# Optimization experiments

Hardware: AMD Instinct MI355X
Metric: run time of the kernel (lower is better)

Reference implementation:

```python
import jax, jax.numpy as jnp
import numpy as np

N = 100000   # total atoms in the batch
E = 400000   # directed edges (bonds both directions)
F = 11       # raw atom feature dim (Linear(11, vector_dim))
D = 512      # vector_dim
L = 5        # num_conv_layers
G = 2048     # number of molecules (graphs) in the batch


def setup_inputs() -> dict:
    key = jax.random.key(0)
    k = jax.random.split(key, 6)
    x = jax.random.uniform(k[0], (N, F), dtype=jnp.float32)  # nonneg counts-like features
    edge_index = jax.random.randint(k[1], (2, E), 0, N, dtype=jnp.int32)
    batch = jnp.sort(jax.random.randint(k[2], (N,), 0, G, dtype=jnp.int32))
    exp_W = jax.random.normal(k[3], (F, D), dtype=jnp.float32) * (1.0 / np.sqrt(F))
    exp_b = jnp.zeros((D,), dtype=jnp.float32)
    gcn_W = jax.random.normal(k[4], (L, D, D), dtype=jnp.float32) * (1.0 / np.sqrt(D))
    gcn_b = jnp.zeros((L, D), dtype=jnp.float32)
    return {"x": x, "edge_index": edge_index, "batch": batch,
            "exp_W": exp_W, "exp_b": exp_b, "gcn_W": gcn_W, "gcn_b": gcn_b}


def reference(x, edge_index, batch, exp_W, exp_b, gcn_W, gcn_b):
    # GraphEmbedding.forward (eval mode: dropout = identity)
    src, dst = edge_index[0], edge_index[1]
    h = jnp.log(x + 1.0) @ exp_W + exp_b  # expansion Linear(11, D)  -> [N, D]

    # GCN normalization with improved=True: self-loop weight 2.0
    # deg_i = sum of incoming edge weights (1.0) + 2.0 self-loop
    ones_e = jnp.ones((E,), dtype=h.dtype)
    deg = jax.ops.segment_sum(ones_e, dst, num_segments=N) + 2.0
    dinv = jax.lax.rsqrt(deg)              # deg >= 2, always finite
    enorm = dinv[src] * dinv[dst]          # per-edge norm (weight 1.0)
    self_norm = 2.0 * dinv * dinv          # self-loop norm (weight 2.0)

    for l in range(L):
        xw = h @ gcn_W[l]                                   # [N, D]
        msg = enorm[:, None] * xw[src]                      # gather + scale, [E, D]
        agg = jax.ops.segment_sum(msg, dst, num_segments=N)  # scatter-add
        agg = agg + self_norm[:, None] * xw + gcn_b[l]
        h = h + jax.nn.relu(agg)                            # residual + relu (dropout off)

    # global_add_pool over molecules
    return jax.ops.segment_sum(h, batch, num_segments=G)    # [G, D]
```

## Files before the change

### kernel.cpp

```cpp
#include <hip/hip_runtime.h>
#include <hip/hip_bf16.h>
#include <stdint.h>

typedef __attribute__((ext_vector_type(8))) short bf16x8;
typedef __attribute__((ext_vector_type(4))) float f32x4;
typedef unsigned short ushort_t;
typedef unsigned int uint_t;

__device__ __forceinline__ unsigned short f2bf(float f) {
  unsigned u = __float_as_uint(f);
  u += 0x7fffu + ((u >> 16) & 1u);
  return (unsigned short)(u >> 16);
}
__device__ __forceinline__ float bf2f(unsigned u16) {
  return __uint_as_float(u16 << 16);
}

__global__ void k_zero(int* __restrict__ p, int n) {
  int i = blockIdx.x * blockDim.x + threadIdx.x;
  if (i < n) p[i] = 0;
}

__global__ void k_prep_w(const float* __restrict__ W, ushort_t* __restrict__ Wt, int total) {
  int idx = blockIdx.x * blockDim.x + threadIdx.x;
  if (idx >= total) return;
  int j   = idx & 7;
  int col = (idx >> 3) & 127;
  int kg  = (idx >> 10) & 3;
  int kt  = (idx >> 12) & 15;
  int nt  = (idx >> 16) & 3;
  int l   = idx >> 18;
  int k = kt * 32 + kg * 8 + j;
  int n = nt * 128 + col;
  Wt[idx] = f2bf(W[((size_t)(l * 512 + k)) * 512 + n]);
}

__global__ __launch_bounds__(256) void k_expand(const float* __restrict__ x,
                                                const float* __restrict__ eW,
                                                const float* __restrict__ eb,
                                                ushort_t* __restrict__ h, int N) {
  const int wid = (blockIdx.x * 256 + threadIdx.x) >> 6;
  const int nw = (gridDim.x * 256) >> 6;
  const int l = threadIdx.x & 63;

  float wf[11][8];
  float bias[8];
#pragma unroll
  for (int f = 0; f < 11; ++f) {
    float4 a = *(const float4*)&eW[f * 512 + l * 8];
    float4 b = *(const float4*)&eW[f * 512 + l * 8 + 4];
    wf[f][0] = a.x; wf[f][1] = a.y; wf[f][2] = a.z; wf[f][3] = a.w;
    wf[f][4] = b.x; wf[f][5] = b.y; wf[f][6] = b.z; wf[f][7] = b.w;
  }
  {
    float4 a = *(const float4*)&eb[l * 8];
    float4 b = *(const float4*)&eb[l * 8 + 4];
    bias[0] = a.x; bias[1] = a.y; bias[2] = a.z; bias[3] = a.w;
    bias[4] = b.x; bias[5] = b.y; bias[6] = b.z; bias[7] = b.w;
  }

  for (int n = wid; n < N; n += nw) {
    float xv = (l < 11) ? x[(size_t)n * 11 + l] : 0.f;
    float lx = log1pf(xv);
    float acc[8];
#pragma unroll
    for (int j = 0; j < 8; ++j) acc[j] = bias[j];
#pragma unroll
    for (int f = 0; f < 11; ++f) {
      float c = __shfl(lx, f, 64);
#pragma unroll
      for (int j = 0; j < 8; ++j) acc[j] += c * wf[f][j];
    }
    uint4 pu;
    pu.x = (uint_t)f2bf(acc[0]) | ((uint_t)f2bf(acc[1]) << 16);
    pu.y = (uint_t)f2bf(acc[2]) | ((uint_t)f2bf(acc[3]) << 16);
    pu.z = (uint_t)f2bf(acc[4]) | ((uint_t)f2bf(acc[5]) << 16);
    pu.w = (uint_t)f2bf(acc[6]) | ((uint_t)f2bf(acc[7]) << 16);
    *(uint4*)(h + (size_t)n * 512 + l * 8) = pu;
  }
}

__global__ void k_deg(const int* __restrict__ dst, int* __restrict__ deg, int E) {
  int e = blockIdx.x * blockDim.x + threadIdx.x;
  if (e < E) atomicAdd(&deg[dst[e]], 1);
}

__global__ void k_dinv(const int* __restrict__ deg, float* __restrict__ dinv,
                       float* __restrict__ selfn, int N) {
  int n = blockIdx.x * blockDim.x + threadIdx.x;
  if (n >= N) return;
  float d = (float)deg[n] + 2.0f;
  dinv[n] = rsqrtf(d);
  selfn[n] = 2.0f / d;
}

__global__ void k_scan_a(const int* __restrict__ deg, int* __restrict__ off,
                         int* __restrict__ bsum, int N) {
  __shared__ int sd[256];
  int t = threadIdx.x;
  int i0 = blockIdx.x * 1024 + t * 4;
  int d[4];
#pragma unroll
  for (int j = 0; j < 4; ++j) d[j] = (i0 + j < N) ? deg[i0 + j] : 0;
  int ts = d[0] + d[1] + d[2] + d[3];
  sd[t] = ts;
  __syncthreads();
  for (int o = 1; o < 256; o <<= 1) {
    int v = (t >= o) ? sd[t - o] : 0;
    __syncthreads();
    sd[t] += v;
    __syncthreads();
  }
  int incl = sd[t];
  int run = incl - ts;
#pragma unroll
  for (int j = 0; j < 4; ++j) {
    if (i0 + j < N) off[i0 + j] = run;
    run += d[j];
  }
  if (t == 255) bsum[blockIdx.x] = incl;
}

__global__ void k_scan_b(const int* __restrict__ bsum, int* __restrict__ bpre, int nb,
                         int* __restrict__ off, int N, int E) {
  __shared__ int sd[256];
  int t = threadIdx.x;
  int v = (t < nb) ? bsum[t] : 0;
  sd[t] = v;
  __syncthreads();
  for (int o = 1; o < 256; o <<= 1) {
    int u = (t >= o) ? sd[t - o] : 0;
    __syncthreads();
    sd[t] += u;
    __syncthreads();
  }
  if (t < nb) bpre[t] = sd[t] - v;
  if (t == 0) off[N] = E;
}

__global__ void k_scan_c(int* __restrict__ off, const int* __restrict__ bpre, int N) {
  int i = blockIdx.x * blockDim.x + threadIdx.x;
  if (i < N) off[i] += bpre[i >> 10];
}

__global__ void k_fill(const int* __restrict__ src, const int* __restrict__ dst,
                       const int* __restrict__ off, int* __restrict__ cur,
                       int* __restrict__ ssrc, int E) {
  int e = blockIdx.x * blockDim.x + threadIdx.x;
  if (e >= E) return;
  int t = dst[e];
  int p = atomicAdd(&cur[t], 1);
  ssrc[off[t] + p] = src[e];
}

__global__ __launch_bounds__(256) void k_agg2(const ushort_t* __restrict__ h,
                                              ushort_t* __restrict__ s,
                                              const int* __restrict__ off,
                                              const int* __restrict__ ssrc,
                                              const float* __restrict__ dinv,
                                              const float* __restrict__ selfn, int N) {
  const int wid = (blockIdx.x * 256 + threadIdx.x) >> 6;
  const int nw = (gridDim.x * 256) >> 6;
  const int l = threadIdx.x & 63;

  for (int n = wid; n < N; n += nw) {
    int s0 = off[n], s1 = off[n + 1];
    float dn = dinv[n];
    float sn = selfn[n];
    float acc[8];
    {
      uint4 u = *(const uint4*)(h + (size_t)n * 512 + l * 8);
      acc[0] = sn * bf2f(u.x & 0xffffu); acc[1] = sn * bf2f(u.x >> 16);
      acc[2] = sn * bf2f(u.y & 0xffffu); acc[3] = sn * bf2f(u.y >> 16);
      acc[4] = sn * bf2f(u.z & 0xffffu); acc[5] = sn * bf2f(u.z >> 16);
      acc[6] = sn * bf2f(u.w & 0xffffu); acc[7] = sn * bf2f(u.w >> 16);
    }
    for (int i = s0; i < s1; ++i) {
      int sv = ssrc[i];
      float w = dn * dinv[sv];
      uint4 u = *(const uint4*)(h + (size_t)sv * 512 + l * 8);
      acc[0] += w * bf2f(u.x & 0xffffu); acc[1] += w * bf2f(u.x >> 16);
      acc[2] += w * bf2f(u.y & 0xffffu); acc[3] += w * bf2f(u.y >> 16);
      acc[4] += w * bf2f(u.z & 0xffffu); acc[5] += w * bf2f(u.z >> 16);
      acc[6] += w * bf2f(u.w & 0xffffu); acc[7] += w * bf2f(u.w >> 16);
    }
    uint4 pu;
    pu.x = (uint_t)f2bf(acc[0]) | ((uint_t)f2bf(acc[1]) << 16);
    pu.y = (uint_t)f2bf(acc[2]) | ((uint_t)f2bf(acc[3]) << 16);
    pu.z = (uint_t)f2bf(acc[4]) | ((uint_t)f2bf(acc[5]) << 16);
    pu.w = (uint_t)f2bf(acc[6]) | ((uint_t)f2bf(acc[7]) << 16);
    *(uint4*)(s + (size_t)n * 512 + l * 8) = pu;
  }
}

__global__ __launch_bounds__(256) void k_gemm(const ushort_t* __restrict__ s,
                                              const ushort_t* __restrict__ Wt,
                                              const float* __restrict__ gbl,
                                              ushort_t* __restrict__ h, int N) {
  __shared__ alignas(16) short Alds[4 * 128 * 8];
  __shared__ alignas(16) short Blds[4 * 128 * 8];
  const int tid = threadIdx.x;
  const int m0 = blockIdx.x * 128;
  const int nt = blockIdx.y;
  const int wv = tid >> 6, ln = tid & 63;
  const int wrow = wv >> 1, wcol = wv & 1;
  const int l15 = ln & 15, l4 = ln >> 4;

  f32x4 acc[4][4];
#pragma unroll
  for (int i = 0; i < 4; ++i)
#pragma unroll
    for (int j = 0; j < 4; ++j) acc[i][j] = (f32x4){0.f, 0.f, 0.f, 0.f};

  const int r = tid >> 1, hh = tid & 1;
  const int grow = m0 + r;
  const bool valid = grow < N;
  const ushort_t* srow = s + (size_t)grow * 512 + hh * 16;
  const int abase0 = ((hh * 2 + 0) * 128 + r) * 8;
  const int abase1 = ((hh * 2 + 1) * 128 + r) * 8;

  for (int kt = 0; kt < 16; ++kt) {
    __syncthreads();
    {
      const ushort_t* wt = Wt + (((size_t)nt * 16 + kt) << 12);
      const ushort_t* g1 = wt + ((wv * 64 + ln) << 3);
      const ushort_t* g2 = g1 + 2048;
      __builtin_amdgcn_global_load_lds(
          (const __attribute__((address_space(1))) unsigned int*)g1,
          (__attribute__((address_space(3))) unsigned int*)&Blds[(wv * 64) << 3], 16, 0, 0);
      __builtin_amdgcn_global_load_lds(
          (const __attribute__((address_space(1))) unsigned int*)g2,
          (__attribute__((address_space(3))) unsigned int*)&Blds[(256 + wv * 64) << 3], 16, 0, 0);
    }
    {
      bf16x8 v0, v1;
      if (valid) {
        v0 = ((const bf16x8*)(srow + kt * 32))[0];
        v1 = ((const bf16x8*)(srow + kt * 32))[1];
      } else {
        v0 = (bf16x8){0, 0, 0, 0, 0, 0, 0, 0};
        v1 = v0;
      }
      *(bf16x8*)&Alds[abase0] = v0;
      *(bf16x8*)&Alds[abase1] = v1;
    }
    __syncthreads();
    bf16x8 a[4], b[4];
#pragma unroll
    for (int i = 0; i < 4; ++i) {
      a[i] = *(const bf16x8*)&Alds[(l4 * 128 + wrow * 64 + i * 16 + l15) * 8];
      b[i] = *(const bf16x8*)&Blds[(l4 * 128 + wcol * 64 + i * 16 + l15) * 8];
    }
#pragma unroll
    for (int i = 0; i < 4; ++i)
#pragma unroll
      for (int j = 0; j < 4; ++j)
        acc[i][j] = __builtin_amdgcn_mfma_f32_16x16x32_bf16(a[i], b[j], acc[i][j], 0, 0, 0);
  }

  float bj[4];
#pragma unroll
  for (int j = 0; j < 4; ++j)
    bj[j] = gbl[nt * 128 + wcol * 64 + j * 16 + l15];

#pragma unroll
  for (int i = 0; i < 4; ++i) {
    int row0 = m0 + wrow * 64 + i * 16 + l4 * 4;
#pragma unroll
    for (int v = 0; v < 4; ++v) {
      int row = row0 + v;
      if (row < N) {
#pragma unroll
        for (int j = 0; j < 4; ++j) {
          int col = nt * 128 + wcol * 64 + j * 16 + l15;
          size_t idx = (size_t)row * 512 + col;
          float hv = bf2f(h[idx]);
          hv += fmaxf(acc[i][j][v] + bj[j], 0.f);
          h[idx] = f2bf(hv);
        }
      }
    }
  }
}

__device__ __forceinline__ int lbound(const int* a, int n, int v) {
  int lo = 0, hi = n;
  while (lo < hi) {
    int m = (lo + hi) >> 1;
    if (a[m] < v) lo = m + 1; else hi = m;
  }
  return lo;
}

__global__ __launch_bounds__(256) void k_pool(const ushort_t* __restrict__ h,
                                              const int* __restrict__ batch,
                                              float* __restrict__ out, int N) {
  __shared__ float red[4 * 512];
  int g = blockIdx.x;
  int t = threadIdx.x;
  int w = t >> 6, l = t & 63;
  int start = lbound(batch, N, g);
  int end = lbound(batch, N, g + 1);
  float acc[8];
#pragma unroll
  for (int j = 0; j < 8; ++j) acc[j] = 0.f;
  for (int n = start + w; n < end; n += 4) {
    uint4 u = *(const uint4*)(h + (size_t)n * 512 + l * 8);
    acc[0] += bf2f(u.x & 0xffffu); acc[1] += bf2f(u.x >> 16);
    acc[2] += bf2f(u.y & 0xffffu); acc[3] += bf2f(u.y >> 16);
    acc[4] += bf2f(u.z & 0xffffu); acc[5] += bf2f(u.z >> 16);
    acc[6] += bf2f(u.w & 0xffffu); acc[7] += bf2f(u.w >> 16);
  }
#pragma unroll
  for (int j = 0; j < 8; ++j) red[w * 512 + l * 8 + j] = acc[j];
  __syncthreads();
  if (t < 128) {
    float4 sv = make_float4(0.f, 0.f, 0.f, 0.f);
#pragma unroll
    for (int ww = 0; ww < 4; ++ww) {
      float4 v = *(const float4*)&red[ww * 512 + t * 4];
      sv.x += v.x; sv.y += v.y; sv.z += v.z; sv.w += v.w;
    }
    *(float4*)&out[(size_t)g * 512 + t * 4] = sv;
  }
}

extern "C" void kernel_launch(void* const* d_in, const int* in_sizes, int n_in,
                              void* d_out, int out_size, void* d_ws, size_t ws_size,
                              hipStream_t stream) {
  const float* x  = (const float*)d_in[0];
  const int* ei   = (const int*)d_in[1];
  const int* batch= (const int*)d_in[2];
  const float* eW = (const float*)d_in[3];
  const float* eb = (const float*)d_in[4];
  const float* gW = (const float*)d_in[5];
  const float* gb = (const float*)d_in[6];
  float* out = (float*)d_out;

  const int N = in_sizes[0] / 11;
  const int E = in_sizes[1] / 2;
  const int G = out_size / 512;
  const int L = in_sizes[5] / (512 * 512);

  const int* src = ei;
  const int* dst = ei + E;

  size_t nd = (size_t)N * 512;
  char* p = (char*)d_ws;
  auto carve = [&](size_t bytes) {
    char* q = p;
    p += (bytes + 255) & ~(size_t)255;
    return q;
  };
  ushort_t* h         = (ushort_t*)carve(nd * 2);
  ushort_t* s         = (ushort_t*)carve(nd * 2);
  ushort_t* Wt        = (ushort_t*)carve((size_t)L * 512 * 512 * 2);
  int* deg            = (int*)carve((size_t)N * 4);
  float* dinv         = (float*)carve((size_t)N * 4);
  float* selfn        = (float*)carve((size_t)N * 4);
  int* off            = (int*)carve(((size_t)N + 1) * 4);
  int* cur            = (int*)carve((size_t)N * 4);
  int* ssrc           = (int*)carve((size_t)E * 4);
  int* bsum           = (int*)carve(1024);
  int* bpre           = (int*)carve(1024);

  k_zero<<<(N + 255) / 256, 256, 0, stream>>>(deg, N);
  k_zero<<<(N + 255) / 256, 256, 0, stream>>>(cur, N);

  int totW = L * 512 * 512;
  k_prep_w<<<(totW + 255) / 256, 256, 0, stream>>>(gW, Wt, totW);
  k_expand<<<2048, 256, 0, stream>>>(x, eW, eb, h, N);
  k_deg<<<(E + 255) / 256, 256, 0, stream>>>(dst, deg, E);
  k_dinv<<<(N + 255) / 256, 256, 0, stream>>>(deg, dinv, selfn, N);
  int nb = (N + 1023) / 1024;
  k_scan_a<<<nb, 256, 0, stream>>>(deg, off, bsum, N);
  k_scan_b<<<1, 256, 0, stream>>>(bsum, bpre, nb, off, N, E);
  k_scan_c<<<(N + 255) / 256, 256, 0, stream>>>(off, bpre, N);
  k_fill<<<(E + 255) / 256, 256, 0, stream>>>(src, dst, off, cur, ssrc, E);

  dim3 ggrid((N + 127) / 128, 4);
  for (int l = 0; l < L; ++l) {
    k_agg2<<<2048, 256, 0, stream>>>(h, s, off, ssrc, dinv, selfn, N);
    k_gemm<<<ggrid, 256, 0, stream>>>(s, Wt + (size_t)l * 512 * 512,
                                      gb + (size_t)l * 512, h, N);
  }
  k_pool<<<G, 256, 0, stream>>>(h, batch, out, N);
}
```

Before: 1.172 ms.

## Interleave two nodes in aggregation, async-load A tiles, stage GEMM epilogue via LDS

The aggregation kernel now has each wavefront handle two destination nodes at once, interleaving their neighbor gathers so more independent loads are in flight. The GEMM loads A tiles with direct global-to-LDS loads in a row-major layout, replacing register staging. Its epilogue writes accumulators to shared memory and then performs coalesced 16-byte read-modify-write of h instead of scattered 2-byte accesses. The costs are extra synchronisation in the epilogue, a different LDS read pattern for A that may cause bank conflicts, and clamped row indices for out-of-range rows.

```diff
diff --git a/kernel.cpp b/kernel.cpp
--- a/kernel.cpp
+++ b/kernel.cpp
@@ -14,6 +14,20 @@
 }
 __device__ __forceinline__ float bf2f(unsigned u16) {
   return __uint_as_float(u16 << 16);
+}
+__device__ __forceinline__ void fma8(float* a, uint4 u, float w) {
+  a[0] += w * bf2f(u.x & 0xffffu); a[1] += w * bf2f(u.x >> 16);
+  a[2] += w * bf2f(u.y & 0xffffu); a[3] += w * bf2f(u.y >> 16);
+  a[4] += w * bf2f(u.z & 0xffffu); a[5] += w * bf2f(u.z >> 16);
+  a[6] += w * bf2f(u.w & 0xffffu); a[7] += w * bf2f(u.w >> 16);
+}
+__device__ __forceinline__ uint4 pack8u(const float* a) {
+  uint4 p;
+  p.x = (uint_t)f2bf(a[0]) | ((uint_t)f2bf(a[1]) << 16);
+  p.y = (uint_t)f2bf(a[2]) | ((uint_t)f2bf(a[3]) << 16);
+  p.z = (uint_t)f2bf(a[4]) | ((uint_t)f2bf(a[5]) << 16);
+  p.w = (uint_t)f2bf(a[6]) | ((uint_t)f2bf(a[7]) << 16);
+  return p;
 }
 
 __global__ void k_zero(int* __restrict__ p, int n) {
@@ -71,12 +85,7 @@
 #pragma unroll
       for (int j = 0; j < 8; ++j) acc[j] += c * wf[f][j];
     }
-    uint4 pu;
-    pu.x = (uint_t)f2bf(acc[0]) | ((uint_t)f2bf(acc[1]) << 16);
-    pu.y = (uint_t)f2bf(acc[2]) | ((uint_t)f2bf(acc[3]) << 16);
-    pu.z = (uint_t)f2bf(acc[4]) | ((uint_t)f2bf(acc[5]) << 16);
-    pu.w = (uint_t)f2bf(acc[6]) | ((uint_t)f2bf(acc[7]) << 16);
-    *(uint4*)(h + (size_t)n * 512 + l * 8) = pu;
+    *(uint4*)(h + (size_t)n * 512 + l * 8) = pack8u(acc);
   }
 }
 
@@ -163,33 +172,49 @@
   const int nw = (gridDim.x * 256) >> 6;
   const int l = threadIdx.x & 63;
 
-  for (int n = wid; n < N; n += nw) {
-    int s0 = off[n], s1 = off[n + 1];
-    float dn = dinv[n];
-    float sn = selfn[n];
-    float acc[8];
+  for (int n0 = wid * 2; n0 < N; n0 += nw * 2) {
+    const int n1 = n0 + 1;
+    const bool v1 = n1 < N;
+    int i0 = off[n0], e0 = off[n0 + 1];
+    int i1 = v1 ? e0 : 0, e1 = v1 ? off[n1 + 1] : 0;
+    float dn0 = dinv[n0], dn1 = v1 ? dinv[n1] : 0.f;
+    float a0[8], a1[8];
     {
-      uint4 u = *(const uint4*)(h + (size_t)n * 512 + l * 8);
-      acc[0] = sn * bf2f(u.x & 0xffffu); acc[1] = sn * bf2f(u.x >> 16);
-      acc[2] = sn * bf2f(u.y & 0xffffu); acc[3] = sn * bf2f(u.y >> 16);
-      acc[4] = sn * bf2f(u.z & 0xffffu); acc[5] = sn * bf2f(u.z >> 16);
-      acc[6] = sn * bf2f(u.w & 0xffffu); acc[7] = sn * bf2f(u.w >> 16);
-    }
-    for (int i = s0; i < s1; ++i) {
-      int sv = ssrc[i];
-      float w = dn * dinv[sv];
-      uint4 u = *(const uint4*)(h + (size_t)sv * 512 + l * 8);
-      acc[0] += w * bf2f(u.x & 0xffffu); acc[1] += w * bf2f(u.x >> 16);
-      acc[2] += w * bf2f(u.y & 0xffffu); acc[3] += w * bf2f(u.y >> 16);
-      acc[4] += w * bf2f(u.z & 0xffffu); acc[5] += w * bf2f(u.z >> 16);
-      acc[6] += w * bf2f(u.w & 0xffffu); acc[7] += w * bf2f(u.w >> 16);
-    }
-    uint4 pu;
-    pu.x = (uint_t)f2bf(acc[0]) | ((uint_t)f2bf(acc[1]) << 16);
-    pu.y = (uint_t)f2bf(acc[2]) | ((uint_t)f2bf(acc[3]) << 16);
-    pu.z = (uint_t)f2bf(acc[4]) | ((uint_t)f2bf(acc[5]) << 16);
-    pu.w = (uint_t)f2bf(acc[6]) | ((uint_t)f2bf(acc[7]) << 16);
-    *(uint4*)(s + (size_t)n * 512 + l * 8) = pu;
+      uint4 u = *(const uint4*)(h + (size_t)n0 * 512 + l * 8);
+      float sn = selfn[n0];
+      a0[0] = sn * bf2f(u.x & 0xffffu); a0[1] = sn * bf2f(u.x >> 16);
+      a0[2] = sn * bf2f(u.y & 0xffffu); a0[3] = sn * bf2f(u.y >> 16);
+      a0[4] = sn * bf2f(u.z & 0xffffu); a0[5] = sn * bf2f(u.z >> 16);
+      a0[6] = sn * bf2f(u.w & 0xffffu); a0[7] = sn * bf2f(u.w >> 16);
+    }
+#pragma unroll
+    for (int j = 0; j < 8; ++j) a1[j] = 0.f;
+    if (v1) {
+      uint4 u = *(const uint4*)(h + (size_t)n1 * 512 + l * 8);
+      fma8(a1, u, selfn[n1]);
+    }
+    while (i0 < e0 && i1 < e1) {
+      int m0 = ssrc[i0++], m1 = ssrc[i1++];
+      float w0 = dn0 * dinv[m0], w1 = dn1 * dinv[m1];
+      uint4 u0 = *(const uint4*)(h + (size_t)m0 * 512 + l * 8);
+      uint4 u1 = *(const uint4*)(h + (size_t)m1 * 512 + l * 8);
+      fma8(a0, u0, w0);
+      fma8(a1, u1, w1);
+    }
+    while (i0 < e0) {
+      int m0 = ssrc[i0++];
+      float w0 = dn0 * dinv[m0];
+      uint4 u0 = *(const uint4*)(h + (size_t)m0 * 512 + l * 8);
+      fma8(a0, u0, w0);
+    }
+    while (i1 < e1) {
+      int m1 = ssrc[i1++];
+      float w1 = dn1 * dinv[m1];
+      uint4 u1 = *(const uint4*)(h + (size_t)m1 * 512 + l * 8);
+      fma8(a1, u1, w1);
+    }
+    *(uint4*)(s + (size_t)n0 * 512 + l * 8) = pack8u(a0);
+    if (v1) *(uint4*)(s + (size_t)n1 * 512 + l * 8) = pack8u(a1);
   }
 }
 
@@ -197,8 +222,9 @@
                                               const ushort_t* __restrict__ Wt,
                                               const float* __restrict__ gbl,
                                               ushort_t* __restrict__ h, int N) {
-  __shared__ alignas(16) short Alds[4 * 128 * 8];
-  __shared__ alignas(16) short Blds[4 * 128 * 8];
+  __shared__ alignas(16) ushort_t smem[8192];
+  ushort_t* Alds = smem;
+  ushort_t* Blds = smem + 4096;
   const int tid = threadIdx.x;
   const int m0 = blockIdx.x * 128;
   const int nt = blockIdx.y;
@@ -212,45 +238,40 @@
 #pragma unroll
     for (int j = 0; j < 4; ++j) acc[i][j] = (f32x4){0.f, 0.f, 0.f, 0.f};
 
-  const int r = tid >> 1, hh = tid & 1;
-  const int grow = m0 + r;
-  const bool valid = grow < N;
-  const ushort_t* srow = s + (size_t)grow * 512 + hh * 16;
-  const int abase0 = ((hh * 2 + 0) * 128 + r) * 8;
-  const int abase1 = ((hh * 2 + 1) * 128 + r) * 8;
+  const int arow0 = tid >> 2, apiece = tid & 3;
+  const int grow0 = min(m0 + arow0, N - 1);
+  const int grow1 = min(m0 + 64 + arow0, N - 1);
 
   for (int kt = 0; kt < 16; ++kt) {
     __syncthreads();
+    {
+      const ushort_t* p0 = s + (size_t)grow0 * 512 + kt * 32 + apiece * 8;
+      const ushort_t* p1 = s + (size_t)grow1 * 512 + kt * 32 + apiece * 8;
+      __builtin_amdgcn_global_load_lds(
+          (const __attribute__((address_space(1))) uint_t*)p0,
+          (__attribute__((address_space(3))) uint_t*)&Alds[tid * 8], 16, 0, 0);
+      __builtin_amdgcn_global_load_lds(
+          (const __attribute__((address_space(1))) uint_t*)p1,
+          (__attribute__((address_space(3))) uint_t*)&Alds[(256 + tid) * 8], 16, 0, 0);
+    }
     {
       const ushort_t* wt = Wt + (((size_t)nt * 16 + kt) << 12);
-      const ushort_t* g1 = wt + ((wv * 64 + ln) << 3);
-      const ushort_t* g2 = g1 + 2048;
+      const ushort_t* g1 = wt + (tid << 3);
       __builtin_amdgcn_global_load_lds(
-          (const __attribute__((address_space(1))) unsigned int*)g1,
-          (__attribute__((address_space(3))) unsigned int*)&Blds[(wv * 64) << 3], 16, 0, 0);
+          (const __attribute__((address_space(1))) uint_t*)g1,
+          (__attribute__((address_space(3))) uint_t*)&Blds[tid * 8], 16, 0, 0);
       __builtin_amdgcn_global_load_lds(
-          (const __attribute__((address_space(1))) unsigned int*)g2,
-          (__attribute__((address_space(3))) unsigned int*)&Blds[(256 + wv * 64) << 3], 16, 0, 0);
-    }
-    {
-      bf16x8 v0, v1;
-      if (valid) {
-        v0 = ((const bf16x8*)(srow + kt * 32))[0];
-        v1 = ((const bf16x8*)(srow + kt * 32))[1];
-      } else {
-        v0 = (bf16x8){0, 0, 0, 0, 0, 0, 0, 0};
-        v1 = v0;
-      }
-      *(bf16x8*)&Alds[abase0] = v0;
-      *(bf16x8*)&Alds[abase1] = v1;
+          (const __attribute__((address_space(1))) uint_t*)(g1 + 2048),
+          (__attribute__((address_space(3))) uint_t*)&Blds[(256 + tid) * 8], 16, 0, 0);
     }
     __syncthreads();
     bf16x8 a[4], b[4];
 #pragma unroll
-    for (int i = 0; i < 4; ++i) {
-      a[i] = *(const bf16x8*)&Alds[(l4 * 128 + wrow * 64 + i * 16 + l15) * 8];
-      b[i] = *(const bf16x8*)&Blds[(l4 * 128 + wcol * 64 + i * 16 + l15) * 8];
-    }
+    for (int i = 0; i < 4; ++i)
+      a[i] = *(const bf16x8*)&Alds[(wrow * 64 + i * 16 + l15) * 32 + l4 * 8];
+#pragma unroll
+    for (int j = 0; j < 4; ++j)
+      b[j] = *(const bf16x8*)&Blds[(l4 * 128 + wcol * 64 + j * 16 + l15) * 8];
 #pragma unroll
     for (int i = 0; i < 4; ++i)
 #pragma unroll
@@ -258,28 +279,51 @@
         acc[i][j] = __builtin_amdgcn_mfma_f32_16x16x32_bf16(a[i], b[j], acc[i][j], 0, 0, 0);
   }
 
-  float bj[4];
-#pragma unroll
-  for (int j = 0; j < 4; ++j)
-    bj[j] = gbl[nt * 128 + wcol * 64 + j * 16 + l15];
-
-#pragma unroll
-  for (int i = 0; i < 4; ++i) {
-    int row0 = m0 + wrow * 64 + i * 16 + l4 * 4;
-#pragma unroll
-    for (int v = 0; v < 4; ++v) {
-      int row = row0 + v;
-      if (row < N) {
-#pragma unroll
-        for (int j = 0; j < 4; ++j) {
-          int col = nt * 128 + wcol * 64 + j * 16 + l15;
-          size_t idx = (size_t)row * 512 + col;
-          float hv = bf2f(h[idx]);
-          hv += fmaxf(acc[i][j][v] + bj[j], 0.f);
-          h[idx] = f2bf(hv);
+  float* cst = (float*)smem;
+  __syncthreads();
+#pragma unroll
+  for (int p = 0; p < 4; ++p) {
+    const int wrow_sel = p >> 1, ipair = (p & 1) * 2;
+    if (wrow == wrow_sel) {
+#pragma unroll
+      for (int ii = 0; ii < 2; ++ii) {
+        int i = ipair + ii;
+#pragma unroll
+        for (int v = 0; v < 4; ++v) {
+          int r32 = ii * 16 + l4 * 4 + v;
+#pragma unroll
+          for (int j = 0; j < 4; ++j)
+            cst[r32 * 128 + wcol * 64 + j * 16 + l15] = acc[i][j][v];
         }
       }
     }
+    __syncthreads();
+#pragma unroll
+    for (int k = 0; k < 2; ++k) {
+      int u = k * 256 + tid;
+      int row_l = u >> 4, cb = u & 15;
+      int grow = m0 + wrow_sel * 64 + ipair * 16 + row_l;
+      if (grow < N) {
+        float4 c0 = *(const float4*)&cst[row_l * 128 + cb * 8];
+        float4 c1 = *(const float4*)&cst[row_l * 128 + cb * 8 + 4];
+        float c[8] = {c0.x, c0.y, c0.z, c0.w, c1.x, c1.y, c1.z, c1.w};
+        const float* gp = gbl + nt * 128 + cb * 8;
+        float4 b0 = *(const float4*)gp;
+        float4 b1 = *(const float4*)(gp + 4);
+        float bb[8] = {b0.x, b0.y, b0.z, b0.w, b1.x, b1.y, b1.z, b1.w};
+        ushort_t* hp = h + (size_t)grow * 512 + nt * 128 + cb * 8;
+        uint4 hu = *(const uint4*)hp;
+        float hv[8];
+        hv[0] = bf2f(hu.x & 0xffffu); hv[1] = bf2f(hu.x >> 16);
+        hv[2] = bf2f(hu.y & 0xffffu); hv[3] = bf2f(hu.y >> 16);
+        hv[4] = bf2f(hu.z & 0xffffu); hv[5] = bf2f(hu.z >> 16);
+        hv[6] = bf2f(hu.w & 0xffffu); hv[7] = bf2f(hu.w >> 16);
+#pragma unroll
+        for (int j = 0; j < 8; ++j) hv[j] += fmaxf(c[j] + bb[j], 0.f);
+        *(uint4*)hp = pack8u(hv);
+      }
+    }
+    __syncthreads();
   }
 }
 
@@ -345,15 +389,14 @@
   const int* src = ei;
   const int* dst = ei + E;
 
-  size_t nd = (size_t)N * 512;
   char* p = (char*)d_ws;
   auto carve = [&](size_t bytes) {
     char* q = p;
     p += (bytes + 255) & ~(size_t)255;
     return q;
   };
-  ushort_t* h         = (ushort_t*)carve(nd * 2);
-  ushort_t* s         = (ushort_t*)carve(nd * 2);
+  ushort_t* h         = (ushort_t*)carve((size_t)N * 512 * 2);
+  ushort_t* s         = (ushort_t*)carve((size_t)N * 512 * 2);
   ushort_t* Wt        = (ushort_t*)carve((size_t)L * 512 * 512 * 2);
   int* deg            = (int*)carve((size_t)N * 4);
   float* dinv         = (float*)carve((size_t)N * 4);
```

New measurement: 1.237 ms. 1.06x slower.
